# Optimization experiments

Hardware: AMD Instinct MI355X
Metric: run time of the kernel (lower is better)

The kernel has to match this reference:

```python
import jax, jax.numpy as jnp
import numpy as np
from jax import lax

B, T, F_IN = 128, 2048, 8
CF = 128   # cnn_filters
H = 96     # lstm_hidden
NC = 6

def _ln(x, g, b, eps=1e-5):
    m = jnp.mean(x, -1, keepdims=True)
    v = jnp.mean((x - m) ** 2, -1, keepdims=True)
    return (x - m) * lax.rsqrt(v + eps) * g + b

def _bn(x, g, b, m, v, eps=1e-5):
    # eval-mode BatchNorm; x is [B,C,T] (channel axis 1) or [B,C]
    if x.ndim == 3:
        return (x - m[None, :, None]) * lax.rsqrt(v + eps)[None, :, None] * g[None, :, None] + b[None, :, None]
    return (x - m) * lax.rsqrt(v + eps) * g + b

def _lstm_scan(xp, whh, bhh, g_hh, b_hh, g_ho, b_ho):
    # xp: [T, B, 4H] = ln_ih(x @ W_ih.T + b_ih), precomputed (LN is per-timestep)
    bsz = xp.shape[1]
    hh = whh.shape[1]
    def step(carry, xt):
        hx, cx = carry
        gates = xt + _ln(hx @ whh.T + bhh, g_hh, b_hh)
        i, f, g, o = jnp.split(gates, 4, axis=-1)  # torch chunk order: in, forget, cell, out
        cy = jax.nn.sigmoid(f) * cx + jax.nn.sigmoid(i) * jnp.tanh(g)
        hy = jax.nn.sigmoid(o) * jnp.tanh(_ln(cy, g_ho, b_ho))
        return (hy, cy), hy
    init = (jnp.zeros((bsz, hh), xp.dtype), jnp.zeros((bsz, hh), xp.dtype))
    _, hs = lax.scan(step, init, xp)
    return hs  # [T, B, H]

def setup_inputs():
    key = jax.random.key(0)
    ks = iter(jax.random.split(key, 64))
    def rn(shape, scale=1.0):
        return jax.random.normal(next(ks), shape, jnp.float32) * scale
    def ru(shape, lo, hi):
        return jax.random.uniform(next(ks), shape, jnp.float32, lo, hi)
    D = 2 * CF  # lstm input size = 256
    d = {}
    d['x'] = rn((B, T, F_IN))
    d['conv1_w'] = rn((CF, F_IN, 7), 1.0 / np.sqrt(F_IN * 7)); d['conv1_b'] = jnp.zeros((CF,))
    d['bn1_g'] = jnp.ones((CF,)); d['bn1_b'] = jnp.zeros((CF,))
    d['bn1_m'] = rn((CF,), 0.1); d['bn1_v'] = ru((CF,), 0.5, 1.5)
    d['conv2_w'] = rn((2 * CF, CF, 5), 1.0 / np.sqrt(CF * 5)); d['conv2_b'] = jnp.zeros((2 * CF,))
    d['bn2_g'] = jnp.ones((2 * CF,)); d['bn2_b'] = jnp.zeros((2 * CF,))
    d['bn2_m'] = rn((2 * CF,), 0.1); d['bn2_v'] = ru((2 * CF,), 0.5, 1.5)
    s = 1.0 / np.sqrt(H)
    for p in ['f', 'b']:
        d[p + 'wih'] = rn((4 * H, D), s); d[p + 'bih'] = rn((4 * H,), s)
        d[p + 'whh'] = rn((4 * H, H), s); d[p + 'bhh'] = rn((4 * H,), s)
        d[p + 'lnih_g'] = jnp.ones((4 * H,)); d[p + 'lnih_b'] = jnp.zeros((4 * H,))
        d[p + 'lnhh_g'] = jnp.ones((4 * H,)); d[p + 'lnhh_b'] = jnp.zeros((4 * H,))
        d[p + 'lnho_g'] = jnp.ones((H,)); d[p + 'lnho_b'] = jnp.zeros((H,))
    d['attn_w'] = rn((1, 2 * H), 1.0 / np.sqrt(2 * H))
    d['fc1_w'] = rn((256, 2 * H), 1.0 / np.sqrt(2 * H)); d['fc1_b'] = jnp.zeros((256,))
    d['bn3_g'] = jnp.ones((256,)); d['bn3_b'] = jnp.zeros((256,))
    d['bn3_m'] = rn((256,), 0.1); d['bn3_v'] = ru((256,), 0.5, 1.5)
    d['fc2_w'] = rn((NC, 256), 1.0 / np.sqrt(256)); d['fc2_b'] = jnp.zeros((NC,))
    return d

def _forward(x, conv1_w, conv1_b, bn1_g, bn1_b, bn1_m, bn1_v,
             conv2_w, conv2_b, bn2_g, bn2_b, bn2_m, bn2_v,
             fwih, fbih, fwhh, fbhh, flnih_g, flnih_b, flnhh_g, flnhh_b, flnho_g, flnho_b,
             bwih, bbih, bwhh, bbhh, blnih_g, blnih_b, blnhh_g, blnhh_b, blnho_g, blnho_b,
             attn_w, fc1_w, fc1_b, bn3_g, bn3_b, bn3_m, bn3_v, fc2_w, fc2_b):
    dn = ('NCH', 'OIH', 'NCH')
    h = jnp.transpose(x, (0, 2, 1))  # [B, F_IN, T]
    h = lax.conv_general_dilated(h, conv1_w, (1,), [(3, 3)], dimension_numbers=dn) + conv1_b[None, :, None]
    h = jax.nn.relu(_bn(h, bn1_g, bn1_b, bn1_m, bn1_v))
    h = lax.reduce_window(h, -jnp.inf, lax.max, (1, 1, 2), (1, 1, 2), 'VALID')
    h = lax.conv_general_dilated(h, conv2_w, (1,), [(2, 2)], dimension_numbers=dn) + conv2_b[None, :, None]
    h = jax.nn.relu(_bn(h, bn2_g, bn2_b, bn2_m, bn2_v))
    h = lax.reduce_window(h, -jnp.inf, lax.max, (1, 1, 2), (1, 1, 2), 'VALID')
    # Dropout(0.3) -> identity at eval
    seq = jnp.transpose(h, (2, 0, 1))  # [T/4, B, 2*CF]
    xp_f = _ln(seq @ fwih.T + fbih, flnih_g, flnih_b)
    hf = _lstm_scan(xp_f, fwhh, fbhh, flnhh_g, flnhh_b, flnho_g, flnho_b)
    xp_b = _ln(seq @ bwih.T + bbih, blnih_g, blnih_b)[::-1]
    hb = _lstm_scan(xp_b, bwhh, bbhh, blnhh_g, blnhh_b, blnho_g, blnho_b)[::-1]
    lstm_out = jnp.transpose(jnp.concatenate([hf, hb], -1), (1, 0, 2))  # [B, T/4, 2H]
    attn = jax.nn.softmax(lstm_out @ attn_w.T, axis=1)  # [B, T/4, 1]
    ctx = jnp.sum(attn * lstm_out, axis=1)  # [B, 2H]
    h2 = jax.nn.relu(_bn(ctx @ fc1_w.T + fc1_b, bn3_g, bn3_b, bn3_m, bn3_v))
    return h2 @ fc2_w.T + fc2_b  # [B, NC]

def reference(x, conv1_w, conv1_b, bn1_g, bn1_b, bn1_m, bn1_v,
              conv2_w, conv2_b, bn2_g, bn2_b, bn2_m, bn2_v,
              fwih, fbih, fwhh, fbhh, flnih_g, flnih_b, flnhh_g, flnhh_b, flnho_g, flnho_b,
              bwih, bbih, bwhh, bbhh, blnih_g, blnih_b, blnhh_g, blnhh_b, blnho_g, blnho_b,
              attn_w, fc1_w, fc1_b, bn3_g, bn3_b, bn3_m, bn3_v, fc2_w, fc2_b):
    return _forward(x, conv1_w, conv1_b, bn1_g, bn1_b, bn1_m, bn1_v,
                    conv2_w, conv2_b, bn2_g, bn2_b, bn2_m, bn2_v,
                    fwih, fbih, fwhh, fbhh, flnih_g, flnih_b, flnhh_g, flnhh_b, flnho_g, flnho_b,
                    bwih, bbih, bwhh, bbhh, blnih_g, blnih_b, blnhh_g, blnhh_b, blnho_g, blnho_b,
                    attn_w, fc1_w, fc1_b, bn3_g, bn3_b, bn3_m, bn3_v, fc2_w, fc2_b)
```

## Files before the change

kernel.cpp:

```cpp
#include <hip/hip_runtime.h>

typedef unsigned short u16;
typedef unsigned int   u32;
typedef __attribute__((ext_vector_type(8))) short bf16x8;
typedef __attribute__((ext_vector_type(4))) float f32x4;

#define DI __device__ __forceinline__

DI float b2f(u16 u){ union{u32 i; float f;} x; x.i = ((u32)u)<<16; return x.f; }
DI u16 f2bf(float f){ union{float f; u32 i;} x; x.f=f; u32 r = x.i + 0x7FFFu + ((x.i>>16)&1u); return (u16)(r>>16); }
DI float sigf(float x){ return 1.0f/(1.0f + __expf(-x)); }
DI float tanh_(float x){ return 1.0f - 2.0f/(__expf(2.0f*x)+1.0f); }
DI float dot4(float4 a, float4 b){ return a.x*b.x + a.y*b.y + a.z*b.z + a.w*b.w; }

__global__ __launch_bounds__(256) void k_conv1(
    const float* __restrict__ x, const float* __restrict__ w,
    const float* __restrict__ cb, const float* __restrict__ bg, const float* __restrict__ bb,
    const float* __restrict__ bm, const float* __restrict__ bv, u16* __restrict__ out)
{
  __shared__ __align__(16) float xs[262*8];
  __shared__ __align__(16) float wl[128*7*8];
  __shared__ float As[128], Ss[128];
  const int tid = threadIdx.x;
  const int tc  = blockIdx.x;
  const int b   = blockIdx.y;
  const int tau0 = tc*256;
  for(int f = tid; f < 262*8; f += 256){
    int tt = f >> 3;
    int ci = f & 7;
    int xg = tau0 - 3 + tt;
    float val = 0.f;
    if(xg >= 0 && xg < 2048) val = x[(b*2048 + xg)*8 + ci];
    xs[f] = val;
  }
  for(int d = tid; d < 128*7*8; d += 256){
    int co = d / 56; int r = d - co*56; int k = r >> 3; int ci = r & 7;
    wl[d] = w[(co*8 + ci)*7 + k];
  }
  if(tid < 128){
    float a = bg[tid] * rsqrtf(bv[tid] + 1e-5f);
    As[tid] = a;
    Ss[tid] = (cb[tid] - bm[tid])*a + bb[tid];
  }
  __syncthreads();
  const float4* xs4 = (const float4*)xs;
  const float4* wl4 = (const float4*)wl;
  for(int i = 0; i < 64; i++){
    int idx = i*256 + tid;
    int co = idx >> 7, p = idx & 127;
    float4 xa[8], xb[8];
    #pragma unroll
    for(int d=0; d<8; d++){ xa[d] = xs4[(2*p + d)*2]; xb[d] = xs4[(2*p + d)*2 + 1]; }
    float a0 = 0.f, a1 = 0.f;
    #pragma unroll
    for(int k=0;k<7;k++){
      float4 wa = wl4[(co*7+k)*2], wb = wl4[(co*7+k)*2+1];
      a0 += dot4(xa[k],   wa) + dot4(xb[k],   wb);
      a1 += dot4(xa[k+1], wa) + dot4(xb[k+1], wb);
    }
    float Ac = As[co], Sc = Ss[co];
    float y = fmaxf(fmaxf(a0*Ac+Sc, a1*Ac+Sc), 0.f);
    out[((b*128 + co)<<10) + tc*128 + p] = f2bf(y);
  }
}

__global__ __launch_bounds__(256) void k_prep(
    const float* __restrict__ w, u16* __restrict__ wp3)
{
  const int f = blockIdx.x*256 + threadIdx.x;
  const int co = f / 640; const int r = f - co*640;
  const int ci = r / 5;   const int k = r - ci*5;
  const float wv = w[f];
  const u16 h0 = f2bf(wv);
  const float r1 = wv - b2f(h0);
  const u16 h1 = f2bf(r1);
  const float r2 = r1 - b2f(h1);
  const u16 h2 = f2bf(r2);
  const int cib = ci >> 5, cl = ci & 31;
  const int base = (k*4 + cib)*10240 + co*40 + cl;
  wp3[base]                = h0;
  wp3[base +   5*4*10240]  = h1;
  wp3[base + 2*5*4*10240]  = h2;
}

__global__ __launch_bounds__(512) void k_conv2(
    const u16* __restrict__ cin, const u16* __restrict__ wp3,
    const float* __restrict__ cb, const float* __restrict__ bg, const float* __restrict__ bb,
    const float* __restrict__ bm, const float* __restrict__ bv, u16* __restrict__ seq)
{
  __shared__ __align__(16) u16 xsT[68*136];
  __shared__ __align__(16) u16 wb[3][256*40];
  __shared__ float As[256], Ss[256];
  const int tid = threadIdx.x;
  const int tc  = blockIdx.x;
  const int b   = blockIdx.y;
  const int wav = tid >> 6;
  const int rt  = wav & 3;
  const int coh = wav >> 2;
  const int l = tid & 63;
  const int g = l >> 4;
  const int c = l & 15;
  if(tid < 256){
    float a = bg[tid] * rsqrtf(bv[tid] + 1e-5f);
    As[tid] = a; Ss[tid] = (cb[tid] - bm[tid])*a + bb[tid];
  }
  for(int f = tid; f < 8704; f += 512){
    int ci = f / 68, tt = f - ci*68;
    int tg = tc*64 - 2 + tt;
    u16 val = 0;
    if(tg >= 0 && tg < 1024) val = cin[((b*128 + ci)<<10) + tg];
    xsT[tt*136 + ci] = val;
  }
  f32x4 acc[8];
  #pragma unroll
  for(int n=0;n<8;n++) acc[n] = (f32x4){0.f,0.f,0.f,0.f};
  for(int s=0; s<20; s++){
    const int k = s >> 2, cib = s & 3;
    __syncthreads();
    #pragma unroll
    for(int sp=0; sp<3; sp++){
      const uint4* src = (const uint4*)(wp3 + ((sp*5 + k)*4 + cib)*10240);
      uint4* dst = (uint4*)wb[sp];
      for(int f = tid; f < 1280; f += 512) dst[f] = src[f];
    }
    __syncthreads();
    bf16x8 afr = *(const bf16x8*)&xsT[(rt*16 + c + k)*136 + cib*32 + g*8];
    #pragma unroll
    for(int n=0; n<8; n++){
      bf16x8 b0 = *(const bf16x8*)&wb[0][(coh*128 + n*16 + c)*40 + g*8];
      bf16x8 b1 = *(const bf16x8*)&wb[1][(coh*128 + n*16 + c)*40 + g*8];
      bf16x8 b2 = *(const bf16x8*)&wb[2][(coh*128 + n*16 + c)*40 + g*8];
      acc[n] = __builtin_amdgcn_mfma_f32_16x16x32_bf16(afr, b0, acc[n], 0, 0, 0);
      acc[n] = __builtin_amdgcn_mfma_f32_16x16x32_bf16(afr, b1, acc[n], 0, 0, 0);
      acc[n] = __builtin_amdgcn_mfma_f32_16x16x32_bf16(afr, b2, acc[n], 0, 0, 0);
    }
  }
  const int tp0 = tc*32 + rt*8 + g*2;
  #pragma unroll
  for(int n=0; n<8; n++){
    int co = coh*128 + n*16 + c;
    float Ac = As[co], Sc = Ss[co];
    float p0 = fmaxf(fmaxf(acc[n][0]*Ac+Sc, acc[n][1]*Ac+Sc), 0.f);
    float p1 = fmaxf(fmaxf(acc[n][2]*Ac+Sc, acc[n][3]*Ac+Sc), 0.f);
    seq[((tp0+0)*128 + b)*256 + co] = f2bf(p0);
    seq[((tp0+1)*128 + b)*256 + co] = f2bf(p1);
  }
}

__global__ __launch_bounds__(512) void k_xp(
    const u16* __restrict__ seq,
    const float* __restrict__ fw, const float* __restrict__ fbi, const float* __restrict__ fg, const float* __restrict__ fb,
    const float* __restrict__ bw, const float* __restrict__ bbi, const float* __restrict__ bg_, const float* __restrict__ bb_,
    u16* __restrict__ xpf, u16* __restrict__ xpb)
{
  __shared__ __align__(16) char lds[104960];
  u16*   wbh  = (u16*)lds;
  u16*   wbl  = (u16*)(lds + 30720);
  u16*   ost  = (u16*)lds;
  float* lnbi = (float*)(lds + 100352);
  float* lng  = lnbi + 384;
  float* lnb2 = lnbi + 768;
  const float *W, *BI, *LG, *LB; u16* out;
  if(blockIdx.y == 0){ W=fw; BI=fbi; LG=fg;  LB=fb;  out=xpf; }
  else               { W=bw; BI=bbi; LG=bg_; LB=bb_; out=xpb; }
  const int tid = threadIdx.x;
  const int row0 = blockIdx.x * 128;
  const int w = tid >> 6;
  const int l = tid & 63;
  const int g = l >> 4;
  const int c = l & 15;
  if(tid < 384){ lnbi[tid] = BI[tid]; lng[tid] = LG[tid]; lnb2[tid] = LB[tid]; }
  const int arow = row0 + w*16 + c;
  bf16x8 afr[8];
  #pragma unroll
  for(int ks=0; ks<8; ks++)
    afr[ks] = *(const bf16x8*)&seq[arow*256 + ks*32 + g*8];
  f32x4 acc[24];
  #pragma unroll
  for(int n=0; n<24; n++) acc[n] = (f32x4){0.f,0.f,0.f,0.f};
  #pragma unroll
  for(int ks=0; ks<8; ks++){
    __syncthreads();
    for(int f = tid; f < 12288; f += 512){
      int jj = f >> 5, kk = f & 31;
      float wv = W[jj*256 + ks*32 + kk];
      u16 hi = f2bf(wv);
      wbh[jj*40 + kk] = hi;
      wbl[jj*40 + kk] = f2bf(wv - b2f(hi));
    }
    __syncthreads();
    #pragma unroll
    for(int n=0; n<24; n++){
      bf16x8 bhi = *(const bf16x8*)&wbh[(n*16 + c)*40 + g*8];
      bf16x8 blo = *(const bf16x8*)&wbl[(n*16 + c)*40 + g*8];
      acc[n] = __builtin_amdgcn_mfma_f32_16x16x32_bf16(afr[ks], bhi, acc[n], 0, 0, 0);
      acc[n] = __builtin_amdgcn_mfma_f32_16x16x32_bf16(afr[ks], blo, acc[n], 0, 0, 0);
    }
  }
  __syncthreads();
  float bic[24];
  #pragma unroll
  for(int n=0; n<24; n++) bic[n] = lnbi[n*16 + c];
  float mean[4], rs[4];
  #pragma unroll
  for(int q=0; q<4; q++){
    float s = 0.f, ss = 0.f;
    #pragma unroll
    for(int n=0; n<24; n++){
      float u = acc[n][q] + bic[n];
      s += u; ss += u*u;
    }
    #pragma unroll
    for(int msk=1; msk<16; msk<<=1){ s += __shfl_xor(s,msk); ss += __shfl_xor(ss,msk); }
    mean[q] = s * (1.f/384.f);
    float var = fmaxf(ss * (1.f/384.f) - mean[q]*mean[q], 0.f);
    rs[q] = rsqrtf(var + 1e-5f);
  }
  #pragma unroll
  for(int n=0; n<24; n++){
    float lgv = lng[n*16 + c], lbv = lnb2[n*16 + c];
    #pragma unroll
    for(int q=0; q<4; q++){
      float u = acc[n][q] + bic[n];
      float y = (u - mean[q])*rs[q]*lgv + lbv;
      ost[(w*16 + g*4 + q)*392 + n*16 + c] = f2bf(y);
    }
  }
  __syncthreads();
  for(int f = tid; f < 6144; f += 512){
    int row = f / 48, ch = f - row*48;
    uint4 v = *(const uint4*)&ost[row*392 + ch*8];
    *(uint4*)&out[(row0 + row)*384 + ch*8] = v;
  }
}

__global__ __launch_bounds__(384) void k_lstm(
    const u16* __restrict__ xpf, const u16* __restrict__ xpb,
    const float* __restrict__ fwhh, const float* __restrict__ fbhh, const float* __restrict__ fgh, const float* __restrict__ fbh2,
    const float* __restrict__ fgho, const float* __restrict__ fbho,
    const float* __restrict__ bwhh, const float* __restrict__ bbhh, const float* __restrict__ bgh, const float* __restrict__ bbh2,
    const float* __restrict__ bgho, const float* __restrict__ bbho,
    u16* __restrict__ hcat)
{
  __shared__ float4 hx4[24];
  __shared__ float gbuf[384];
  __shared__ float red[16];
  const int b   = blockIdx.x;
  const int dir = blockIdx.y;
  const u16* xp;
  const float *whh, *bh, *gh, *bh2, *gho, *bho;
  if(dir == 0){ xp=xpf; whh=fwhh; bh=fbhh; gh=fgh; bh2=fbh2; gho=fgho; bho=fbho; }
  else        { xp=xpb; whh=bwhh; bh=bbhh; gh=bgh; bh2=bbh2; gho=bgho; bho=bbho; }
  const int j = threadIdx.x;
  const int wid = j >> 6;
  float wr[96];
  {
    const float4* wp4 = (const float4*)(whh + j*96);
    #pragma unroll
    for(int kk=0; kk<24; kk++){
      float4 v = wp4[kk];
      wr[4*kk]=v.x; wr[4*kk+1]=v.y; wr[4*kk+2]=v.z; wr[4*kk+3]=v.w;
    }
  }
  const float bh_j = bh[j], gh_j = gh[j], bh2_j = bh2[j];
  float gho_j = 0.f, bho_j = 0.f, cx = 0.f;
  if(j < 96){ gho_j = gho[j]; bho_j = bho[j]; }
  float* hx = (float*)hx4;
  if(j < 96) hx[j] = 0.f;
  __syncthreads();
  for(int t=0; t<512; t++){
    const int ts = dir ? (511 - t) : t;
    const float xt = b2f(xp[(ts*128 + b)*384 + j]);
    float a0=0.f,a1=0.f,a2=0.f,a3=0.f;
    #pragma unroll
    for(int kk=0; kk<24; kk++){
      float4 h4 = hx4[kk];
      a0 += h4.x * wr[4*kk];
      a1 += h4.y * wr[4*kk+1];
      a2 += h4.z * wr[4*kk+2];
      a3 += h4.w * wr[4*kk+3];
    }
    const float u = (a0+a1)+(a2+a3) + bh_j;
    float s = u, ss = u*u;
    #pragma unroll
    for(int msk=32; msk; msk>>=1){ s += __shfl_xor(s,msk); ss += __shfl_xor(ss,msk); }
    if((j & 63) == 0){ red[wid*2] = s; red[wid*2+1] = ss; }
    __syncthreads();
    float S=0.f, SS=0.f;
    #pragma unroll
    for(int wv=0; wv<6; wv++){ S += red[wv*2]; SS += red[wv*2+1]; }
    const float mean = S*(1.f/384.f);
    const float var  = fmaxf(SS*(1.f/384.f) - mean*mean, 0.f);
    const float rs   = rsqrtf(var + 1e-5f);
    const float gate = xt + (u - mean)*rs*gh_j + bh2_j;
    gbuf[j] = gate;
    __syncthreads();
    float cy = 0.f, go_ = 0.f;
    if(j < 128){
      if(j < 96){
        float gi = gbuf[j], gf = gbuf[j+96], gg = gbuf[j+192];
        go_ = gbuf[j+288];
        cy = sigf(gf)*cx + sigf(gi)*tanh_(gg);
        cx = cy;
      }
      float s2 = cy, ss2 = cy*cy;
      #pragma unroll
      for(int msk=32; msk; msk>>=1){ s2 += __shfl_xor(s2,msk); ss2 += __shfl_xor(ss2,msk); }
      if((j & 63) == 0){ red[12 + wid*2] = s2; red[13 + wid*2] = ss2; }
    }
    __syncthreads();
    if(j < 96){
      const float S2 = red[12]+red[14], SS2 = red[13]+red[15];
      const float m2  = S2*(1.f/96.f);
      const float v2  = fmaxf(SS2*(1.f/96.f) - m2*m2, 0.f);
      const float rs2 = rsqrtf(v2 + 1e-5f);
      const float lnho = (cy - m2)*rs2*gho_j + bho_j;
      const float hy = sigf(go_)*tanh_(lnho);
      hx[j] = hy;
      hcat[(ts*128 + b)*192 + dir*96 + j] = f2bf(hy);
    }
    __syncthreads();
  }
}

__global__ __launch_bounds__(256) void k_head(
    const u16* __restrict__ hcat, const float* __restrict__ aw,
    const float* __restrict__ f1w, const float* __restrict__ f1b,
    const float* __restrict__ g3, const float* __restrict__ b3, const float* __restrict__ m3, const float* __restrict__ v3,
    const float* __restrict__ fc2w, const float* __restrict__ fc2bias,
    float* __restrict__ out)
{
  __shared__ float p[512];
  __shared__ float red[8];
  __shared__ __align__(16) float ctx[192];
  __shared__ float h2[256];
  __shared__ float awl[192];
  const int b = blockIdx.x;
  const int tid = threadIdx.x;
  if(tid < 192) awl[tid] = aw[tid];
  __syncthreads();
  float sc0 = 0.f, sc1 = 0.f;
  #pragma unroll
  for(int i=0;i<2;i++){
    int t = i*256 + tid;
    const uint4* hp = (const uint4*)(hcat + (t*128 + b)*192);
    float acc = 0.f;
    #pragma unroll 6
    for(int qq=0;qq<24;qq++){
      uint4 pv = hp[qq];
      acc += b2f((u16)(pv.x&0xffffu))*awl[qq*8+0] + b2f((u16)(pv.x>>16))*awl[qq*8+1]
           + b2f((u16)(pv.y&0xffffu))*awl[qq*8+2] + b2f((u16)(pv.y>>16))*awl[qq*8+3]
           + b2f((u16)(pv.z&0xffffu))*awl[qq*8+4] + b2f((u16)(pv.z>>16))*awl[qq*8+5]
           + b2f((u16)(pv.w&0xffffu))*awl[qq*8+6] + b2f((u16)(pv.w>>16))*awl[qq*8+7];
    }
    if(i==0) sc0 = acc; else sc1 = acc;
  }
  float mx = fmaxf(sc0, sc1);
  for(int msk=32; msk; msk>>=1) mx = fmaxf(mx, __shfl_xor(mx,msk));
  if((tid&63)==0) red[tid>>6] = mx;
  __syncthreads();
  mx = fmaxf(fmaxf(red[0],red[1]), fmaxf(red[2],red[3]));
  float e0 = __expf(sc0-mx), e1 = __expf(sc1-mx);
  float sm = e0 + e1;
  for(int msk=32; msk; msk>>=1) sm += __shfl_xor(sm,msk);
  if((tid&63)==0) red[4 + (tid>>6)] = sm;
  __syncthreads();
  const float inv = 1.f/(red[4]+red[5]+red[6]+red[7]);
  p[tid] = e0*inv; p[tid+256] = e1*inv;
  __syncthreads();
  if(tid < 192){
    float acc = 0.f;
    for(int t=0;t<512;t++){
      acc += p[t] * b2f(hcat[(t*128 + b)*192 + tid]);
    }
    ctx[tid] = acc;
  }
  __syncthreads();
  {
    const float4* cv = (const float4*)ctx;
    const float4* wp = (const float4*)(f1w + tid*192);
    float acc = 0.f;
    #pragma unroll 8
    for(int qq=0;qq<48;qq++){
      acc += dot4(wp[qq], cv[qq]);
    }
    acc += f1b[tid];
    float a = g3[tid] * rsqrtf(v3[tid] + 1e-5f);
    float y = (acc - m3[tid])*a + b3[tid];
    h2[tid] = fmaxf(y, 0.f);
  }
  __syncthreads();
  if(tid < 6){
    float acc = fc2bias[tid];
    for(int k=0;k<256;k++) acc += h2[k]*fc2w[tid*256 + k];
    out[b*6 + tid] = acc;
  }
}

extern "C" void kernel_launch(void* const* d_in, const int* in_sizes, int n_in,
                              void* d_out, int out_size, void* d_ws, size_t ws_size,
                              hipStream_t stream)
{
  (void)in_sizes; (void)n_in; (void)out_size; (void)ws_size;
  const float* X      = (const float*)d_in[0];
  const float* c1w    = (const float*)d_in[1];
  const float* c1b    = (const float*)d_in[2];
  const float* bn1g   = (const float*)d_in[3];
  const float* bn1b   = (const float*)d_in[4];
  const float* bn1m   = (const float*)d_in[5];
  const float* bn1v   = (const float*)d_in[6];
  const float* c2w    = (const float*)d_in[7];
  const float* c2b    = (const float*)d_in[8];
  const float* bn2g   = (const float*)d_in[9];
  const float* bn2b   = (const float*)d_in[10];
  const float* bn2m   = (const float*)d_in[11];
  const float* bn2v   = (const float*)d_in[12];
  const float* fwih   = (const float*)d_in[13];
  const float* fbih   = (const float*)d_in[14];
  const float* fwhh   = (const float*)d_in[15];
  const float* fbhh   = (const float*)d_in[16];
  const float* flnihg = (const float*)d_in[17];
  const float* flnihb = (const float*)d_in[18];
  const float* flnhhg = (const float*)d_in[19];
  const float* flnhhb = (const float*)d_in[20];
  const float* flnhog = (const float*)d_in[21];
  const float* flnhob = (const float*)d_in[22];
  const float* bwih   = (const float*)d_in[23];
  const float* bbih   = (const float*)d_in[24];
  const float* bwhh   = (const float*)d_in[25];
  const float* bbhh   = (const float*)d_in[26];
  const float* blnihg = (const float*)d_in[27];
  const float* blnihb = (const float*)d_in[28];
  const float* blnhhg = (const float*)d_in[29];
  const float* blnhhb = (const float*)d_in[30];
  const float* blnhog = (const float*)d_in[31];
  const float* blnhob = (const float*)d_in[32];
  const float* attnw  = (const float*)d_in[33];
  const float* fc1w   = (const float*)d_in[34];
  const float* fc1b   = (const float*)d_in[35];
  const float* bn3g   = (const float*)d_in[36];
  const float* bn3b   = (const float*)d_in[37];
  const float* bn3m   = (const float*)d_in[38];
  const float* bn3v   = (const float*)d_in[39];
  const float* fc2w   = (const float*)d_in[40];
  const float* fc2b_  = (const float*)d_in[41];

  char* ws = (char*)d_ws;
  const size_t MB = 1048576;
  u16* seq   = (u16*)(ws);
  u16* xpf   = (u16*)(ws + 32*MB);
  u16* xpb   = (u16*)(ws + 80*MB);
  u16* wprep = (u16*)(ws + 80*MB);
  u16* c1o   = (u16*)(ws + 96*MB);
  u16* hcat  = (u16*)(ws);

  k_prep <<<dim3(640),    256, 0, stream>>>(c2w, wprep);
  k_conv1<<<dim3(8,128),  256, 0, stream>>>(X,   c1w, c1b, bn1g, bn1b, bn1m, bn1v, c1o);
  k_conv2<<<dim3(16,128), 512, 0, stream>>>(c1o, wprep, c2b, bn2g, bn2b, bn2m, bn2v, seq);
  k_xp  <<<dim3(512,2),   512, 0, stream>>>(seq, fwih, fbih, flnihg, flnihb,
                                                 bwih, bbih, blnihg, blnihb, xpf, xpb);
  k_lstm<<<dim3(128,2),   384, 0, stream>>>(xpf, xpb,
      fwhh, fbhh, flnhhg, flnhhb, flnhog, flnhob,
      bwhh, bbhh, blnhhg, blnhhb, blnhog, blnhob, hcat);
  k_head<<<dim3(128),     256, 0, stream>>>(hcat, attnw, fc1w, fc1b,
      bn3g, bn3b, bn3m, bn3v, fc2w, fc2b_, (float*)d_out);
}
```

Before: 1.733 ms.

## Register-block conv1 over time and enlarge conv2 time tile for weight reuse

Conv1 now has each thread hold a sliding window of 10 input rows in registers and compute 4 adjacent outputs (2 pooled) for 32 output channels. It writes packed bf16 pairs, and the input LDS rows are padded to 12 floats. Conv2 now covers 4x more timesteps per block with 4 accumulator sets, so each staged weight tile in LDS feeds 4x more MFMAs and the grid shrinks from 16x128 to 4x128 blocks. The cost is higher register and LDS use, which lowers occupancy, and fewer blocks for conv2.

```diff
diff --git a/kernel.cpp b/kernel.cpp
--- a/kernel.cpp
+++ b/kernel.cpp
@@ -18,7 +18,7 @@
     const float* __restrict__ cb, const float* __restrict__ bg, const float* __restrict__ bb,
     const float* __restrict__ bm, const float* __restrict__ bv, u16* __restrict__ out)
 {
-  __shared__ __align__(16) float xs[262*8];
+  __shared__ __align__(16) float xs[262*12];
   __shared__ __align__(16) float wl[128*7*8];
   __shared__ float As[128], Ss[128];
   const int tid = threadIdx.x;
@@ -31,7 +31,7 @@
     int xg = tau0 - 3 + tt;
     float val = 0.f;
     if(xg >= 0 && xg < 2048) val = x[(b*2048 + xg)*8 + ci];
-    xs[f] = val;
+    xs[tt*12 + ci] = val;
   }
   for(int d = tid; d < 128*7*8; d += 256){
     int co = d / 56; int r = d - co*56; int k = r >> 3; int ci = r & 7;
@@ -45,22 +45,27 @@
   __syncthreads();
   const float4* xs4 = (const float4*)xs;
   const float4* wl4 = (const float4*)wl;
-  for(int i = 0; i < 64; i++){
-    int idx = i*256 + tid;
-    int co = idx >> 7, p = idx & 127;
-    float4 xa[8], xb[8];
-    #pragma unroll
-    for(int d=0; d<8; d++){ xa[d] = xs4[(2*p + d)*2]; xb[d] = xs4[(2*p + d)*2 + 1]; }
-    float a0 = 0.f, a1 = 0.f;
+  const int p2  = tid & 63;
+  const int grp = tid >> 6;
+  float4 ra[10], rb[10];
+  #pragma unroll
+  for(int e=0; e<10; e++){ ra[e] = xs4[(4*p2+e)*3]; rb[e] = xs4[(4*p2+e)*3 + 1]; }
+  u32* out32 = (u32*)out;
+  for(int i = 0; i < 32; i++){
+    const int co = grp*32 + i;
+    float a0=0.f, a1=0.f, a2=0.f, a3=0.f;
     #pragma unroll
     for(int k=0;k<7;k++){
-      float4 wa = wl4[(co*7+k)*2], wb = wl4[(co*7+k)*2+1];
-      a0 += dot4(xa[k],   wa) + dot4(xb[k],   wb);
-      a1 += dot4(xa[k+1], wa) + dot4(xb[k+1], wb);
-    }
-    float Ac = As[co], Sc = Ss[co];
-    float y = fmaxf(fmaxf(a0*Ac+Sc, a1*Ac+Sc), 0.f);
-    out[((b*128 + co)<<10) + tc*128 + p] = f2bf(y);
+      float4 wa = wl4[(co*7+k)*2], wb2 = wl4[(co*7+k)*2+1];
+      a0 += dot4(ra[k],   wa) + dot4(rb[k],   wb2);
+      a1 += dot4(ra[k+1], wa) + dot4(rb[k+1], wb2);
+      a2 += dot4(ra[k+2], wa) + dot4(rb[k+2], wb2);
+      a3 += dot4(ra[k+3], wa) + dot4(rb[k+3], wb2);
+    }
+    const float Ac = As[co], Sc = Ss[co];
+    const float y0 = fmaxf(fmaxf(a0*Ac+Sc, a1*Ac+Sc), 0.f);
+    const float y1 = fmaxf(fmaxf(a2*Ac+Sc, a3*Ac+Sc), 0.f);
+    out32[((b*128 + co)<<9) + tc*64 + p2] = (u32)f2bf(y0) | ((u32)f2bf(y1) << 16);
   }
 }
 
@@ -88,7 +93,7 @@
     const float* __restrict__ cb, const float* __restrict__ bg, const float* __restrict__ bb,
     const float* __restrict__ bm, const float* __restrict__ bv, u16* __restrict__ seq)
 {
-  __shared__ __align__(16) u16 xsT[68*136];
+  __shared__ __align__(16) u16 xsT[260*136];
   __shared__ __align__(16) u16 wb[3][256*40];
   __shared__ float As[256], Ss[256];
   const int tid = threadIdx.x;
@@ -104,16 +109,18 @@
     float a = bg[tid] * rsqrtf(bv[tid] + 1e-5f);
     As[tid] = a; Ss[tid] = (cb[tid] - bm[tid])*a + bb[tid];
   }
-  for(int f = tid; f < 8704; f += 512){
-    int ci = f / 68, tt = f - ci*68;
-    int tg = tc*64 - 2 + tt;
+  for(int f = tid; f < 33280; f += 512){
+    int ci = f / 260, tt = f - ci*260;
+    int tg = tc*256 - 2 + tt;
     u16 val = 0;
     if(tg >= 0 && tg < 1024) val = cin[((b*128 + ci)<<10) + tg];
     xsT[tt*136 + ci] = val;
   }
-  f32x4 acc[8];
-  #pragma unroll
-  for(int n=0;n<8;n++) acc[n] = (f32x4){0.f,0.f,0.f,0.f};
+  f32x4 acc[4][8];
+  #pragma unroll
+  for(int q4=0;q4<4;q4++)
+    #pragma unroll
+    for(int n=0;n<8;n++) acc[q4][n] = (f32x4){0.f,0.f,0.f,0.f};
   for(int s=0; s<20; s++){
     const int k = s >> 2, cib = s & 3;
     __syncthreads();
@@ -124,26 +131,36 @@
       for(int f = tid; f < 1280; f += 512) dst[f] = src[f];
     }
     __syncthreads();
-    bf16x8 afr = *(const bf16x8*)&xsT[(rt*16 + c + k)*136 + cib*32 + g*8];
+    bf16x8 afr[4];
+    #pragma unroll
+    for(int q4=0;q4<4;q4++)
+      afr[q4] = *(const bf16x8*)&xsT[((q4*4 + rt)*16 + c + k)*136 + cib*32 + g*8];
     #pragma unroll
     for(int n=0; n<8; n++){
       bf16x8 b0 = *(const bf16x8*)&wb[0][(coh*128 + n*16 + c)*40 + g*8];
       bf16x8 b1 = *(const bf16x8*)&wb[1][(coh*128 + n*16 + c)*40 + g*8];
       bf16x8 b2 = *(const bf16x8*)&wb[2][(coh*128 + n*16 + c)*40 + g*8];
-      acc[n] = __builtin_amdgcn_mfma_f32_16x16x32_bf16(afr, b0, acc[n], 0, 0, 0);
-      acc[n] = __builtin_amdgcn_mfma_f32_16x16x32_bf16(afr, b1, acc[n], 0, 0, 0);
-      acc[n] = __builtin_amdgcn_mfma_f32_16x16x32_bf16(afr, b2, acc[n], 0, 0, 0);
-    }
-  }
-  const int tp0 = tc*32 + rt*8 + g*2;
-  #pragma unroll
-  for(int n=0; n<8; n++){
-    int co = coh*128 + n*16 + c;
-    float Ac = As[co], Sc = Ss[co];
-    float p0 = fmaxf(fmaxf(acc[n][0]*Ac+Sc, acc[n][1]*Ac+Sc), 0.f);
-    float p1 = fmaxf(fmaxf(acc[n][2]*Ac+Sc, acc[n][3]*Ac+Sc), 0.f);
-    seq[((tp0+0)*128 + b)*256 + co] = f2bf(p0);
-    seq[((tp0+1)*128 + b)*256 + co] = f2bf(p1);
+      #pragma unroll
+      for(int q4=0;q4<4;q4++){
+        acc[q4][n] = __builtin_amdgcn_mfma_f32_16x16x32_bf16(afr[q4], b0, acc[q4][n], 0, 0, 0);
+        acc[q4][n] = __builtin_amdgcn_mfma_f32_16x16x32_bf16(afr[q4], b1, acc[q4][n], 0, 0, 0);
+        acc[q4][n] = __builtin_amdgcn_mfma_f32_16x16x32_bf16(afr[q4], b2, acc[q4][n], 0, 0, 0);
+      }
+    }
+  }
+  #pragma unroll
+  for(int q4=0;q4<4;q4++){
+    const int T = q4*4 + rt;
+    const int tp0 = tc*128 + T*8 + g*2;
+    #pragma unroll
+    for(int n=0; n<8; n++){
+      int co = coh*128 + n*16 + c;
+      float Ac = As[co], Sc = Ss[co];
+      float p0 = fmaxf(fmaxf(acc[q4][n][0]*Ac+Sc, acc[q4][n][1]*Ac+Sc), 0.f);
+      float p1 = fmaxf(fmaxf(acc[q4][n][2]*Ac+Sc, acc[q4][n][3]*Ac+Sc), 0.f);
+      seq[((tp0+0)*128 + b)*256 + co] = f2bf(p0);
+      seq[((tp0+1)*128 + b)*256 + co] = f2bf(p1);
+    }
   }
 }
 
@@ -456,7 +473,7 @@
 
   k_prep <<<dim3(640),    256, 0, stream>>>(c2w, wprep);
   k_conv1<<<dim3(8,128),  256, 0, stream>>>(X,   c1w, c1b, bn1g, bn1b, bn1m, bn1v, c1o);
-  k_conv2<<<dim3(16,128), 512, 0, stream>>>(c1o, wprep, c2b, bn2g, bn2b, bn2m, bn2v, seq);
+  k_conv2<<<dim3(4,128),  512, 0, stream>>>(c1o, wprep, c2b, bn2g, bn2b, bn2m, bn2v, seq);
   k_xp  <<<dim3(512,2),   512, 0, stream>>>(seq, fwih, fbih, flnihg, flnihb,
                                                  bwih, bbih, blnihg, blnihb, xpf, xpb);
   k_lstm<<<dim3(128,2),   384, 0, stream>>>(xpf, xpb,
```

After: 1.547 ms. 10.7% less time.
